# Kernel optimization log

Hardware: AMD Instinct MI355X
Metric: run time of the kernel (lower is better)

## Reference

```python
import jax, jax.numpy as jnp
import numpy as np

EPS = 1e-5

def _layernorm(x, g, b):
    # LayerNorm over last dim (head_dim), eps=1e-5 like nn.LayerNorm
    mu = jnp.mean(x, axis=-1, keepdims=True)
    var = jnp.mean(jnp.square(x - mu), axis=-1, keepdims=True)
    return (x - mu) * jax.lax.rsqrt(var + EPS) * g + b

def _rotate_half(x):
    d = x.shape[-1] // 2
    return jnp.concatenate([-x[..., d:], x[..., :d]], axis=-1)

def _apply_rotary(x, cos, sin):
    # x: [B,S,H,D]; cos/sin: [S,D] broadcast over batch and heads
    c = cos[None, :, None, :]
    s = sin[None, :, None, :]
    return x * c + _rotate_half(x) * s

def setup_inputs() -> dict:
    key = jax.random.key(0)
    ks = jax.random.split(key, 16)
    B, S, Dm = 2, 1024, 2048
    H, Hkv, Dh = 16, 4, 128
    f = lambda k, shp: (jax.random.normal(k, shp, dtype=jnp.float32) * 0.02)
    return {
        "hidden_states": jax.random.normal(ks[0], (B, S, Dm), dtype=jnp.float32),
        "cos": jax.random.uniform(ks[1], (S, Dh), dtype=jnp.float32),
        "sin": jax.random.uniform(ks[2], (S, Dh), dtype=jnp.float32),
        "Wq": f(ks[3], (H * Dh, Dm)),   "bq": jnp.zeros((H * Dh,), jnp.float32),
        "Wk": f(ks[4], (Hkv * Dh, Dm)), "bk": jnp.zeros((Hkv * Dh,), jnp.float32),
        "Wv": f(ks[5], (Hkv * Dh, Dm)), "bv": jnp.zeros((Hkv * Dh,), jnp.float32),
        "Wo": f(ks[6], (Dm, H * Dh)),   "bo": jnp.zeros((Dm,), jnp.float32),
        "qn_g": jnp.ones((Dh,), jnp.float32), "qn_b": jnp.zeros((Dh,), jnp.float32),
        "kn_g": jnp.ones((Dh,), jnp.float32), "kn_b": jnp.zeros((Dh,), jnp.float32),
        "cu_seqlens": jnp.array([0, S, 2 * S], dtype=jnp.int32),
        "max_s": 1024,
    }

def reference(hidden_states, cos, sin, Wq, bq, Wk, bk, Wv, bv, Wo, bo,
              qn_g, qn_b, kn_g, kn_b, cu_seqlens, max_s):
    B, S, Dm = hidden_states.shape
    Dh = qn_g.shape[0]
    H = Wq.shape[0] // Dh
    Hkv = Wk.shape[0] // Dh
    scale = 1.0 / jnp.sqrt(jnp.float32(Dh))

    q = (hidden_states @ Wq.T + bq).reshape(B, S, H, Dh)
    k = (hidden_states @ Wk.T + bk).reshape(B, S, Hkv, Dh)
    v = (hidden_states @ Wv.T + bv).reshape(B, S, Hkv, Dh)

    q = _apply_rotary(_layernorm(q, qn_g, qn_b), cos, sin)
    k = _apply_rotary(_layernorm(k, kn_g, kn_b), cos, sin)

    # GQA: repeat_interleave kv heads to match q heads
    n_rep = H // Hkv
    if n_rep > 1:
        k = jnp.repeat(k, n_rep, axis=2)
        v = jnp.repeat(v, n_rep, axis=2)

    # scores: [B,H,S,S]
    scores = jnp.einsum('bqhd,bkhd->bhqk', q, k) * scale
    causal = jnp.tril(jnp.ones((S, S), dtype=bool))
    scores = jnp.where(causal[None, None], scores, jnp.finfo(scores.dtype).min)
    weights = jax.nn.softmax(scores, axis=-1)
    out = jnp.einsum('bhqk,bkhd->bqhd', weights, v).reshape(B, S, H * Dh)
    return out @ Wo.T + bo
```

## Files before the change

kernel.cpp:

```cpp
#include <hip/hip_runtime.h>
#include <cmath>

typedef __attribute__((ext_vector_type(8))) short bf16x8;
typedef __attribute__((ext_vector_type(4))) short s16x4;
typedef __attribute__((ext_vector_type(4))) float f32x4;

#define MFMA_BF16 __builtin_amdgcn_mfma_f32_16x16x32_bf16

__device__ __forceinline__ float bf2f(short s) {
    unsigned u = ((unsigned)(unsigned short)s) << 16;
    return __builtin_bit_cast(float, u);
}
__device__ __forceinline__ short f2bf(float f) {
    unsigned u = __builtin_bit_cast(unsigned, f);
    u += 0x7fffu + ((u >> 16) & 1u);
    return (short)(u >> 16);
}

__device__ __forceinline__ void gl_lds16(const short* gp, short* lp) {
    __builtin_amdgcn_global_load_lds(
        (const __attribute__((address_space(1))) unsigned int*)gp,
        (__attribute__((address_space(3))) unsigned int*)lp, 16, 0, 0);
}

__global__ __launch_bounds__(256) void cvt5(
    const float* s0, short* d0, int n0,
    const float* s1, short* d1, int n1,
    const float* s2, short* d2, int n2,
    const float* s3, short* d3, int n3,
    const float* s4, short* d4, int n4)
{
    long long i = (long long)blockIdx.x * 1024 + threadIdx.x * 4;
    const float* s; short* d;
    if      (i < n0)                  { s = s0; d = d0; }
    else if ((i -= n0) < n1)          { s = s1; d = d1; }
    else if ((i -= n1) < n2)          { s = s2; d = d2; }
    else if ((i -= n2) < n3)          { s = s3; d = d3; }
    else      { i -= n3;                s = s4; d = d4; }
    float4 v = *(const float4*)(s + i);
    s16x4 o;
    o[0] = f2bf(v.x); o[1] = f2bf(v.y); o[2] = f2bf(v.z); o[3] = f2bf(v.w);
    *(s16x4*)(d + i) = o;
}

template <int MODE>
__global__ __launch_bounds__(256) void gemm_t(
    const short* __restrict__ A, const short* __restrict__ W,
    const float* __restrict__ bq, const float* __restrict__ bk,
    const float* __restrict__ bv,
    short* __restrict__ qo, short* __restrict__ ko, short* __restrict__ vo,
    float* __restrict__ fo,
    int M, int K, int S, int Hkv, int Nq, int Nkv, int N)
{
    __shared__ __align__(16) short As[2][2 * 8 * 512];
    __shared__ __align__(16) short Bs[2][2 * 4 * 512];

    const int w    = threadIdx.x >> 6;
    const int lane = threadIdx.x & 63;
    const int l15  = lane & 15;
    const int quad = lane >> 4;
    const int wy   = w >> 1;
    const int wx   = w & 1;
    const int m0   = blockIdx.y * 128;
    const int n0   = blockIdx.x * 64;

    const short* Ab = A + (size_t)m0 * K;
    const short* Wb = W + (size_t)n0 * K;

    const int srow = lane >> 2;
    const int scol = ((lane & 3) ^ ((srow >> 1) & 3)) * 8;
    auto stage = [&](int buf, int kofs) {
#pragma unroll
        for (int h2 = 0; h2 < 2; h2++) {
#pragma unroll
            for (int i = 0; i < 2; i++) {
                const int c = 2 * w + i;
                gl_lds16(Ab + (size_t)(c * 16 + srow) * K + kofs + h2 * 32 + scol,
                         As[buf] + h2 * 4096 + c * 512 + lane * 8);
            }
            gl_lds16(Wb + (size_t)(w * 16 + srow) * K + kofs + h2 * 32 + scol,
                     Bs[buf] + h2 * 2048 + w * 512 + lane * 8);
        }
    };

    f32x4 acc[4][2];
#pragma unroll
    for (int i = 0; i < 4; i++)
#pragma unroll
        for (int j = 0; j < 2; j++) acc[i][j] = f32x4{0.f, 0.f, 0.f, 0.f};

    const int ridx = (l15 * 4 + (quad ^ ((l15 >> 1) & 3))) * 8;
    const int nk = K / 64;
    stage(0, 0);
    __syncthreads();

    for (int kt = 0; kt < nk; kt++) {
        const int cur = kt & 1;
        if (kt + 1 < nk) stage(cur ^ 1, (kt + 1) * 64);

#pragma unroll
        for (int h2 = 0; h2 < 2; h2++) {
            bf16x8 af[4], bfr[2];
#pragma unroll
            for (int i = 0; i < 4; i++)
                af[i] = *(const bf16x8*)(As[cur] + h2 * 4096 + (wy * 4 + i) * 512 + ridx);
#pragma unroll
            for (int j = 0; j < 2; j++)
                bfr[j] = *(const bf16x8*)(Bs[cur] + h2 * 2048 + (wx * 2 + j) * 512 + ridx);
#pragma unroll
            for (int i = 0; i < 4; i++)
#pragma unroll
                for (int j = 0; j < 2; j++)
                    acc[i][j] = MFMA_BF16(af[i], bfr[j], acc[i][j], 0, 0, 0);
        }
        __syncthreads();
    }

#pragma unroll
    for (int i = 0; i < 4; i++) {
#pragma unroll
        for (int j = 0; j < 2; j++) {
            const int col = n0 + wx * 32 + j * 16 + l15;
#pragma unroll
            for (int r = 0; r < 4; r++) {
                const int row = m0 + wy * 64 + i * 16 + quad * 4 + r;
                float v = acc[i][j][r];
                if constexpr (MODE == 0) {
                    if (col < Nq) {
                        qo[(size_t)row * Nq + col] = f2bf(v + bq[col]);
                    } else if (col < Nq + Nkv) {
                        int cn = col - Nq;
                        ko[(size_t)row * Nkv + cn] = f2bf(v + bk[cn]);
                    } else {
                        int cn = col - Nq - Nkv;
                        int b  = row / S, s = row - b * S;
                        int hk = cn >> 7, dh = cn & 127;
                        vo[(size_t)((b * Hkv + hk) * 128 + dh) * S + s] = f2bf(v + bv[cn]);
                    }
                } else {
                    fo[(size_t)row * N + col] = v + bq[col];
                }
            }
        }
    }
}

__global__ __launch_bounds__(256) void ln_rope2(
    const short* __restrict__ Xq, short* __restrict__ Yq,
    const short* __restrict__ Xk, short* __restrict__ Yk,
    const float* __restrict__ qg, const float* __restrict__ qbe,
    const float* __restrict__ kg, const float* __restrict__ kbe,
    const float* __restrict__ cosp, const float* __restrict__ sinp,
    int H, int Hkv, int S, int nq)
{
    int gw = blockIdx.x * 4 + (threadIdx.x >> 6);
    const int lane = threadIdx.x & 63;
    const short* X; short* Y; const float* g; const float* bt; int Hc;
    if (gw < nq) { X = Xq; Y = Yq; g = qg; bt = qbe; Hc = H; }
    else { gw -= nq; X = Xk; Y = Yk; g = kg; bt = kbe; Hc = Hkv; }

    const int h  = gw % Hc;
    const int rs = gw / Hc;
    const int b  = rs / S;
    const int s  = rs - b * S;

    const short* x = X + ((size_t)rs * Hc + h) * 128;
    float x0 = bf2f(x[lane]), x1 = bf2f(x[lane + 64]);

    float sum = x0 + x1;
    float sq  = x0 * x0 + x1 * x1;
#pragma unroll
    for (int off = 32; off > 0; off >>= 1) {
        sum += __shfl_xor(sum, off, 64);
        sq  += __shfl_xor(sq, off, 64);
    }
    float mu  = sum * (1.f / 128.f);
    float var = sq * (1.f / 128.f) - mu * mu;
    float rinv = rsqrtf(var + 1e-5f);

    float y0 = (x0 - mu) * rinv * g[lane]      + bt[lane];
    float y1 = (x1 - mu) * rinv * g[lane + 64] + bt[lane + 64];

    float c0 = cosp[(size_t)s * 128 + lane];
    float c1 = cosp[(size_t)s * 128 + lane + 64];
    float s0 = sinp[(size_t)s * 128 + lane];
    float s1 = sinp[(size_t)s * 128 + lane + 64];

    float o0 = y0 * c0 - y1 * s0;
    float o1 = y1 * c1 + y0 * s1;

    short* yp = Y + ((size_t)(b * Hc + h) * S + s) * 128;
    yp[lane]      = f2bf(o0);
    yp[lane + 64] = f2bf(o1);
}

__global__ __launch_bounds__(256, 2) void attn(
    const short* __restrict__ Q, const short* __restrict__ Kt,
    const short* __restrict__ Vt, short* __restrict__ O,
    int S, int H, int Hkv, int nrep, float scale)
{
    __shared__ __align__(16) short Ks[2][16 * 512];
    __shared__ __align__(16) short Vs[2][16 * 512];
    __shared__ __align__(16) short P[4][16][72];

    const int w    = threadIdx.x >> 6;
    const int lane = threadIdx.x & 63;
    const int l15  = lane & 15;
    const int quad = lane >> 4;
    const int bh   = blockIdx.x;
    const int h    = bh % H;
    const int b    = bh / H;
    const int nyt  = gridDim.y;
    const int y    = blockIdx.y;
    const int qblk = (y < (nyt >> 1)) ? (nyt - 1 - y) : (y - (nyt >> 1));
    const int hk   = h / nrep;
    const int m0   = qblk * 64 + w * 16;
    const int qpos = m0 + l15;

    const short* qb = Q  + (size_t)(b * H + h) * S * 128;
    const short* kb = Kt + (size_t)(b * Hkv + hk) * S * 128;
    const short* vb = Vt + (size_t)(b * Hkv + hk) * 128 * S;

    auto stage = [&](int buf, int j0) {
#pragma unroll
        for (int i = 0; i < 8; i++) {
            if (w < 2) {
                const int s = w * 8 + i;
                const int t = s >> 2, c = s & 3;
                gl_lds16(kb + (size_t)(j0 + t * 16 + l15) * 128 + c * 32 + quad * 8,
                         Ks[buf] + s * 512 + lane * 8);
            } else {
                const int u = (w - 2) * 8 + i;
                const int c = u >> 1, hf = u & 1;
                gl_lds16(vb + (size_t)(c * 16 + l15) * S + j0 + hf * 32 + quad * 8,
                         Vs[buf] + u * 512 + lane * 8);
            }
        }
    };

    bf16x8 qf[4];
#pragma unroll
    for (int c = 0; c < 4; c++)
        qf[c] = *(const bf16x8*)(qb + (size_t)(m0 + l15) * 128 + c * 32 + quad * 8);

    f32x4 of[8];
#pragma unroll
    for (int c = 0; c < 8; c++) of[c] = f32x4{0.f, 0.f, 0.f, 0.f};
    float m_s = -1e30f, l_s = 0.f;
    const float c2 = scale * 1.44269504f;

    const int nkt = qblk + 1;
    stage(0, 0);
    __syncthreads();

    for (int kt = 0; kt < nkt; kt++) {
        const int cur = kt & 1;
        if (kt + 1 < nkt) stage(cur ^ 1, (kt + 1) * 64);

        const short* Kb = Ks[cur];
        const short* Vb = Vs[cur];
        const int j0 = kt * 64;

        f32x4 sc[4];
#pragma unroll
        for (int t = 0; t < 4; t++) sc[t] = f32x4{0.f, 0.f, 0.f, 0.f};
#pragma unroll
        for (int c = 0; c < 4; c++)
#pragma unroll
            for (int t = 0; t < 4; t++) {
                bf16x8 kf = *(const bf16x8*)(Kb + (t * 4 + c) * 512 + lane * 8);
                sc[t] = MFMA_BF16(kf, qf[c], sc[t], 0, 0, 0);
            }

        float v[4][4];
        float mx = -1e30f;
#pragma unroll
        for (int t = 0; t < 4; t++)
#pragma unroll
            for (int r = 0; r < 4; r++) {
                float s_ = sc[t][r];
                if (j0 + t * 16 + quad * 4 + r > qpos) s_ = -1e30f;
                v[t][r] = s_;
                mx = fmaxf(mx, s_);
            }
        mx = fmaxf(mx, __shfl_xor(mx, 16, 64));
        mx = fmaxf(mx, __shfl_xor(mx, 32, 64));
        float mnew  = fmaxf(m_s, mx);
        float mc    = mnew * c2;
        float alpha = exp2f(m_s * c2 - mc);
        float sum = 0.f;
        float p[4][4];
#pragma unroll
        for (int t = 0; t < 4; t++)
#pragma unroll
            for (int r = 0; r < 4; r++) {
                p[t][r] = exp2f(__builtin_fmaf(v[t][r], c2, -mc));
                sum += p[t][r];
            }
        sum += __shfl_xor(sum, 16, 64);
        sum += __shfl_xor(sum, 32, 64);
        l_s = l_s * alpha + sum;
        m_s = mnew;

#pragma unroll
        for (int c = 0; c < 8; c++) {
            f32x4 t = of[c];
            t[0] *= alpha; t[1] *= alpha; t[2] *= alpha; t[3] *= alpha;
            of[c] = t;
        }

#pragma unroll
        for (int t = 0; t < 4; t++) {
            s16x4 pk;
#pragma unroll
            for (int r = 0; r < 4; r++) pk[r] = f2bf(p[t][r]);
            *(s16x4*)(&P[w][l15][t * 16 + quad * 4]) = pk;
        }
        bf16x8 pb0 = *(const bf16x8*)(&P[w][l15][quad * 8]);
        bf16x8 pb1 = *(const bf16x8*)(&P[w][l15][32 + quad * 8]);

#pragma unroll
        for (int c = 0; c < 8; c++) {
            bf16x8 vf0 = *(const bf16x8*)(Vb + (c * 2 + 0) * 512 + lane * 8);
            bf16x8 vf1 = *(const bf16x8*)(Vb + (c * 2 + 1) * 512 + lane * 8);
            of[c] = MFMA_BF16(vf0, pb0, of[c], 0, 0, 0);
            of[c] = MFMA_BF16(vf1, pb1, of[c], 0, 0, 0);
        }
        __syncthreads();
    }

    const int HDh = H * 128;
    const float rinv = 1.0f / l_s;
    short* orow = O + ((size_t)b * S + qpos) * HDh + h * 128;
#pragma unroll
    for (int c = 0; c < 8; c++) {
        s16x4 ov;
#pragma unroll
        for (int r = 0; r < 4; r++) ov[r] = f2bf(of[c][r] * rinv);
        *(s16x4*)(orow + c * 16 + quad * 4) = ov;
    }
}

extern "C" void kernel_launch(void* const* d_in, const int* in_sizes, int n_in,
                              void* d_out, int out_size, void* d_ws, size_t ws_size,
                              hipStream_t stream) {
    const float* hs   = (const float*)d_in[0];
    const float* cosp = (const float*)d_in[1];
    const float* sinp = (const float*)d_in[2];
    const float* Wq   = (const float*)d_in[3];
    const float* bq   = (const float*)d_in[4];
    const float* Wk   = (const float*)d_in[5];
    const float* bk   = (const float*)d_in[6];
    const float* Wv   = (const float*)d_in[7];
    const float* bv   = (const float*)d_in[8];
    const float* Wo   = (const float*)d_in[9];
    const float* bo   = (const float*)d_in[10];
    const float* qg   = (const float*)d_in[11];
    const float* qb_  = (const float*)d_in[12];
    const float* kg   = (const float*)d_in[13];
    const float* kb_  = (const float*)d_in[14];

    const int Dh    = in_sizes[11];
    const int Dm    = in_sizes[10];
    const int HDh   = in_sizes[4];
    const int H     = HDh / Dh;
    const int HkvDh = in_sizes[6];
    const int Hkv   = HkvDh / Dh;
    const int S     = in_sizes[1] / Dh;
    const int B     = in_sizes[0] / (S * Dm);
    const int M     = B * S;
    const int nrep  = H / Hkv;

    char* ws = (char*)d_ws;
    short* hsb  = (short*)ws;  ws += (size_t)M * Dm      * 2;
    short* Wqb  = (short*)ws;  ws += (size_t)HDh * Dm    * 2;
    short* Wkb  = (short*)ws;  ws += (size_t)HkvDh * Dm  * 2;
    short* Wvb  = (short*)ws;  ws += (size_t)HkvDh * Dm  * 2;
    short* Wob  = (short*)ws;  ws += (size_t)Dm * HDh    * 2;
    short* qg16 = (short*)ws;  ws += (size_t)M * HDh     * 2;
    short* kg16 = (short*)ws;  ws += (size_t)M * HkvDh   * 2;
    short* qbuf = (short*)ws;  ws += (size_t)M * HDh     * 2;
    short* kbuf = (short*)ws;  ws += (size_t)M * HkvDh   * 2;
    short* vbuf = (short*)ws;  ws += (size_t)M * HkvDh   * 2;
    short* abuf = qg16;

    dim3 blk(256);
    const int n0 = M * Dm, n1 = HDh * Dm, n2 = HkvDh * Dm, n3 = HkvDh * Dm, n4 = Dm * HDh;
    cvt5<<<dim3((n0 + n1 + n2 + n3 + n4) / 1024), blk, 0, stream>>>(
        hs, hsb, n0, Wq, Wqb, n1, Wk, Wkb, n2, Wv, Wvb, n3, Wo, Wob, n4);

    const int Ntot = HDh + 2 * HkvDh;
    gemm_t<0><<<dim3(Ntot / 64, M / 128), blk, 0, stream>>>(
        hsb, Wqb, bq, bk, bv, qg16, kg16, vbuf, nullptr,
        M, Dm, S, Hkv, HDh, HkvDh, Ntot);

    const int nq = M * H;
    ln_rope2<<<dim3((nq + M * Hkv) / 4), blk, 0, stream>>>(
        qg16, qbuf, kg16, kbuf, qg, qb_, kg, kb_, cosp, sinp, H, Hkv, S, nq);

    const float scale = 1.0f / sqrtf((float)Dh);
    attn<<<dim3(H * B, S / 64), blk, 0, stream>>>(qbuf, kbuf, vbuf, abuf, S, H, Hkv, nrep, scale);

    gemm_t<1><<<dim3(Dm / 64, M / 128), blk, 0, stream>>>(
        abuf, Wob, bo, nullptr, nullptr, nullptr, nullptr, nullptr, (float*)d_out,
        M, HDh, S, Hkv, Dm, 0, Dm);
}
```

Baseline: 242.8 us.

## Add XCD-aware block remapping and a 64x64-tile output projection GEMM

```diff
diff --git a/kernel.cpp b/kernel.cpp
--- a/kernel.cpp
+++ b/kernel.cpp
@@ -61,8 +61,18 @@
     const int quad = lane >> 4;
     const int wy   = w >> 1;
     const int wx   = w & 1;
-    const int m0   = blockIdx.y * 128;
-    const int n0   = blockIdx.x * 64;
+
+    unsigned gx = gridDim.x, gy = gridDim.y;
+    unsigned bx = blockIdx.x, by = blockIdx.y;
+    if ((gx & 3) == 0 && (gy & 1) == 0) {
+        unsigned lin = by * gx + bx;
+        unsigned xcd = lin & 7, idx = lin >> 3;
+        unsigned n   = gx >> 2;
+        bx = (xcd & 3) * n + idx % n;
+        by = (xcd >> 2) * (gy >> 1) + idx / n;
+    }
+    const int m0 = by * 128;
+    const int n0 = bx * 64;
 
     const short* Ab = A + (size_t)m0 * K;
     const short* Wb = W + (size_t)n0 * K;
@@ -125,21 +135,106 @@
             for (int r = 0; r < 4; r++) {
                 const int row = m0 + wy * 64 + i * 16 + quad * 4 + r;
                 float v = acc[i][j][r];
-                if constexpr (MODE == 0) {
-                    if (col < Nq) {
-                        qo[(size_t)row * Nq + col] = f2bf(v + bq[col]);
-                    } else if (col < Nq + Nkv) {
-                        int cn = col - Nq;
-                        ko[(size_t)row * Nkv + cn] = f2bf(v + bk[cn]);
-                    } else {
-                        int cn = col - Nq - Nkv;
-                        int b  = row / S, s = row - b * S;
-                        int hk = cn >> 7, dh = cn & 127;
-                        vo[(size_t)((b * Hkv + hk) * 128 + dh) * S + s] = f2bf(v + bv[cn]);
-                    }
+                if (col < Nq) {
+                    qo[(size_t)row * Nq + col] = f2bf(v + bq[col]);
+                } else if (col < Nq + Nkv) {
+                    int cn = col - Nq;
+                    ko[(size_t)row * Nkv + cn] = f2bf(v + bk[cn]);
                 } else {
-                    fo[(size_t)row * N + col] = v + bq[col];
+                    int cn = col - Nq - Nkv;
+                    int b  = row / S, s = row - b * S;
+                    int hk = cn >> 7, dh = cn & 127;
+                    vo[(size_t)((b * Hkv + hk) * 128 + dh) * S + s] = f2bf(v + bv[cn]);
                 }
+            }
+        }
+    }
+}
+
+__global__ __launch_bounds__(256) void gemm64(
+    const short* __restrict__ A, const short* __restrict__ W,
+    const float* __restrict__ bias, float* __restrict__ out,
+    int K, int N)
+{
+    __shared__ __align__(16) short As[2][2 * 4 * 512];
+    __shared__ __align__(16) short Bs[2][2 * 4 * 512];
+
+    const int w    = threadIdx.x >> 6;
+    const int lane = threadIdx.x & 63;
+    const int l15  = lane & 15;
+    const int quad = lane >> 4;
+    const int wy   = w >> 1;
+    const int wx   = w & 1;
+
+    unsigned gx = gridDim.x, gy = gridDim.y;
+    unsigned bx = blockIdx.x, by = blockIdx.y;
+    if ((gx & 3) == 0 && (gy & 1) == 0) {
+        unsigned lin = by * gx + bx;
+        unsigned xcd = lin & 7, idx = lin >> 3;
+        unsigned n   = gx >> 2;
+        bx = (xcd & 3) * n + idx % n;
+        by = (xcd >> 2) * (gy >> 1) + idx / n;
+    }
+    const int m0 = by * 64;
+    const int n0 = bx * 64;
+
+    const short* Ab = A + (size_t)m0 * K;
+    const short* Wb = W + (size_t)n0 * K;
+
+    const int srow = lane >> 2;
+    const int scol = ((lane & 3) ^ ((srow >> 1) & 3)) * 8;
+    auto stage = [&](int buf, int kofs) {
+#pragma unroll
+        for (int h2 = 0; h2 < 2; h2++) {
+            gl_lds16(Ab + (size_t)(w * 16 + srow) * K + kofs + h2 * 32 + scol,
+                     As[buf] + h2 * 2048 + w * 512 + lane * 8);
+            gl_lds16(Wb + (size_t)(w * 16 + srow) * K + kofs + h2 * 32 + scol,
+                     Bs[buf] + h2 * 2048 + w * 512 + lane * 8);
+        }
+    };
+
+    f32x4 acc[2][2];
+#pragma unroll
+    for (int i = 0; i < 2; i++)
+#pragma unroll
+        for (int j = 0; j < 2; j++) acc[i][j] = f32x4{0.f, 0.f, 0.f, 0.f};
+
+    const int ridx = (l15 * 4 + (quad ^ ((l15 >> 1) & 3))) * 8;
+    const int nk = K / 64;
+    stage(0, 0);
+    __syncthreads();
+
+    for (int kt = 0; kt < nk; kt++) {
+        const int cur = kt & 1;
+        if (kt + 1 < nk) stage(cur ^ 1, (kt + 1) * 64);
+
+#pragma unroll
+        for (int h2 = 0; h2 < 2; h2++) {
+            bf16x8 af[2], bfr[2];
+#pragma unroll
+            for (int i = 0; i < 2; i++)
+                af[i] = *(const bf16x8*)(As[cur] + h2 * 2048 + (wy * 2 + i) * 512 + ridx);
+#pragma unroll
+            for (int j = 0; j < 2; j++)
+                bfr[j] = *(const bf16x8*)(Bs[cur] + h2 * 2048 + (wx * 2 + j) * 512 + ridx);
+#pragma unroll
+            for (int i = 0; i < 2; i++)
+#pragma unroll
+                for (int j = 0; j < 2; j++)
+                    acc[i][j] = MFMA_BF16(af[i], bfr[j], acc[i][j], 0, 0, 0);
+        }
+        __syncthreads();
+    }
+
+#pragma unroll
+    for (int i = 0; i < 2; i++) {
+#pragma unroll
+        for (int j = 0; j < 2; j++) {
+            const int col = n0 + wx * 32 + j * 16 + l15;
+#pragma unroll
+            for (int r = 0; r < 4; r++) {
+                const int row = m0 + wy * 32 + i * 16 + quad * 4 + r;
+                out[(size_t)row * N + col] = acc[i][j][r] + bias[col];
             }
         }
     }
@@ -401,7 +496,6 @@
     const float scale = 1.0f / sqrtf((float)Dh);
     attn<<<dim3(H * B, S / 64), blk, 0, stream>>>(qbuf, kbuf, vbuf, abuf, S, H, Hkv, nrep, scale);
 
-    gemm_t<1><<<dim3(Dm / 64, M / 128), blk, 0, stream>>>(
-        abuf, Wob, bo, nullptr, nullptr, nullptr, nullptr, nullptr, (float*)d_out,
-        M, HDh, S, Hkv, Dm, 0, Dm);
-}
+    gemm64<<<dim3(Dm / 64, M / 64), blk, 0, stream>>>(
+        abuf, Wob, bo, (float*)d_out, HDh, Dm);
+}
```

After: 241.2 us. No clear change (-0.6%).
